# Kernel optimization log

Measured on AMD Instinct MI355X. Metric: run time of the kernel, lower is better.

## Reference

```python
import jax, jax.numpy as jnp
import numpy as np

BITS = 8
EPS = 1e-5
NUM_HEADS = 16


def ste_round(x):
    # straight-through rounding (matches brevitas round STE)
    return x + jax.lax.stop_gradient(jnp.round(x) - x)


def _scale(stat, qmax):
    return jnp.maximum(stat, 1e-8) / qmax


def fq_act_signed(x, bits=BITS):
    # runtime max-abs per-tensor scale (approximates brevitas runtime percentile 99.999)
    qmax = 2 ** (bits - 1) - 1
    qmin = -(2 ** (bits - 1))
    s = _scale(jnp.max(jnp.abs(x)), qmax)
    return jnp.clip(ste_round(x / s), qmin, qmax) * s


def fq_act_unsigned(x, bits=BITS):
    qmax = 2 ** bits - 1
    s = _scale(jnp.max(x), qmax)
    return jnp.clip(ste_round(x / s), 0, qmax) * s


def fq_weight(w, bits=BITS):
    # NarrowIntQuant + MaxStatsScaling: symmetric narrow range [-qmax, qmax]
    qmax = 2 ** (bits - 1) - 1
    s = _scale(jnp.max(jnp.abs(w)), qmax)
    return jnp.clip(ste_round(w / s), -qmax, qmax) * s


def fq_bias(b, bits=BITS):
    qmax = 2 ** (bits - 1) - 1
    qmin = -(2 ** (bits - 1))
    s = _scale(jnp.max(jnp.abs(b)), qmax)
    return jnp.clip(ste_round(b / s), qmin, qmax) * s


def layernorm(x):
    # elementwise_affine=False
    m = jnp.mean(x, axis=-1, keepdims=True)
    v = jnp.mean((x - m) ** 2, axis=-1, keepdims=True)
    return (x - m) / jnp.sqrt(v + EPS)


def setup_inputs() -> dict:
    key = jax.random.key(0)
    ks = jax.random.split(key, 13)
    B, S, E, M = 4, 1024, 1024, 4096
    std = 0.02
    inp = {
        "x": jax.random.normal(ks[0], (B, S, E), jnp.float32),
        "Wq": jax.random.normal(ks[1], (E, E), jnp.float32) * std,
        "bq": jax.random.normal(ks[2], (E,), jnp.float32) * std,
        "Wk": jax.random.normal(ks[3], (E, E), jnp.float32) * std,
        "bk": jax.random.normal(ks[4], (E,), jnp.float32) * std,
        "Wv": jax.random.normal(ks[5], (E, E), jnp.float32) * std,
        "bv": jax.random.normal(ks[6], (E,), jnp.float32) * std,
        "Wo": jax.random.normal(ks[7], (E, E), jnp.float32) * std,
        "bo": jax.random.normal(ks[8], (E,), jnp.float32) * std,
        "W1": jax.random.normal(ks[9], (M, E), jnp.float32) * std,
        "b1": jax.random.normal(ks[10], (M,), jnp.float32) * std,
        "W2": jax.random.normal(ks[11], (E, M), jnp.float32) * std,
        "b2": jax.random.normal(ks[12], (E,), jnp.float32) * std,
    }
    return inp


def reference(x, Wq, bq, Wk, bk, Wv, bv, Wo, bo, W1, b1, W2, b2):
    B, S, E = x.shape
    H = NUM_HEADS
    D = E // H
    # causal additive mask [S, S]
    i = jnp.arange(S)
    mask = jnp.where(i[None, :] <= i[:, None], 0.0, -jnp.inf).astype(x.dtype)

    # sdp_input_quant (shared q=k=v input)
    q_in = fq_act_signed(x)

    # quantized in-proj (packed_in_proj=False -> separate q/k/v projections)
    Q = q_in @ fq_weight(Wq).T + fq_bias(bq)
    K = q_in @ fq_weight(Wk).T + fq_bias(bk)
    V = q_in @ fq_weight(Wv).T + fq_bias(bv)

    Qh = Q.reshape(B, S, H, D)
    Kh = K.reshape(B, S, H, D)
    Vh = V.reshape(B, S, H, D)

    qs = fq_act_signed(Qh / jnp.sqrt(jnp.asarray(D, x.dtype)))  # q_scaled_quant
    kq = fq_act_signed(Kh)  # k_transposed_quant (per-tensor -> transpose-invariant)
    vq = fq_act_signed(Vh)  # v_quant

    scores = jnp.einsum("bqhd,bkhd->bhqk", qs, kq) + mask  # [B,H,S,S]
    attn = fq_act_signed(jax.nn.softmax(scores, axis=-1))  # attn_output_weights_quant

    ctx = jnp.einsum("bhqk,bkhd->bqhd", attn, vq).reshape(B, S, E)
    ctx = fq_act_signed(ctx)  # out_proj_input_quant
    attn_out = ctx @ fq_weight(Wo).T + fq_bias(bo)

    # residual_sdp: QuantEltwiseAdd quantizes both inputs, then layer-norm
    x1 = layernorm(fq_act_signed(x) + fq_act_signed(attn_out))

    # MLP: QuantIdentity -> QuantLinear -> QuantReLU -> QuantLinear
    h = fq_act_signed(x1) @ fq_weight(W1).T + fq_bias(b1)
    h = fq_act_unsigned(jax.nn.relu(h))
    h = h @ fq_weight(W2).T + fq_bias(b2)

    out = layernorm(fq_act_signed(x1) + fq_act_signed(h))
    return out
```

## Files before the change

kernel.cpp:

```cpp
#include <hip/hip_runtime.h>
#include <stdint.h>
#include <stddef.h>


typedef unsigned short u16;
typedef __attribute__((ext_vector_type(4))) int   i32x4;
typedef __attribute__((ext_vector_type(4))) float f32x4;

#define DEV __device__ __forceinline__

DEV float bf2f(u16 u) { return __uint_as_float(((unsigned)u) << 16); }
DEV void atomicMaxF(float* p, float v) { atomicMax((unsigned*)p, __float_as_uint(v)); }
DEV float waveMax(float v) {
#pragma unroll
  for (int o = 32; o; o >>= 1) v = fmaxf(v, __shfl_xor(v, o, 64));
  return v;
}
DEV float waveSum(float v) {
#pragma unroll
  for (int o = 32; o; o >>= 1) v += __shfl_xor(v, o, 64);
  return v;
}
DEV int waveSumI(int v) {
#pragma unroll
  for (int o = 32; o; o >>= 1) v += __shfl_xor(v, o, 64);
  return v;
}
DEV void blockStatMax(float v, float* __restrict__ slot64, float* sred4, int flatBlk) {
  v = waveMax(v);
  const int tid = threadIdx.x;
  if ((tid & 63) == 0) sred4[tid >> 6] = v;
  __syncthreads();
  if (tid == 0) {
    float m = fmaxf(fmaxf(sred4[0], sred4[1]), fmaxf(sred4[2], sred4[3]));
    atomicMaxF(&slot64[flatBlk & 63], m);
  }
}
DEV float slotMax64(const float* __restrict__ s) {
  float m = 0.f;
#pragma unroll
  for (int i = 0; i < 64; ++i) m = fmaxf(m, s[i]);
  return m;
}
DEV f32x4 ld4(const void* p, int i4, int isf32) {
  if (isf32) return ((const f32x4*)p)[i4];
  ushort4 u = ((const ushort4*)p)[i4];
  return (f32x4){bf2f(u.x), bf2f(u.y), bf2f(u.z), bf2f(u.w)};
}
DEV void gll16(const void* g, void* l) {
  __builtin_amdgcn_global_load_lds((__attribute__((address_space(1))) void*)(g),
                                   (__attribute__((address_space(3))) void*)(l),
                                   16, 0, 0);
}
DEV unsigned ldsaddr(const void* p) {
  return (unsigned)(size_t)(__attribute__((address_space(3))) const void*)p;
}
DEV unsigned quadsel(unsigned a, unsigned b, unsigned c, unsigned d, int idx) {
  unsigned lo = (idx & 1) ? b : a;
  unsigned hi = (idx & 1) ? d : c;
  return (idx & 2) ? hi : lo;
}

__global__ void detect_f32(const u16* __restrict__ x, int* __restrict__ flag) {
  const int tid = threadIdx.x;
  int cnt = 0;
#pragma unroll
  for (int i = 0; i < 16; ++i) {
    u16 u = x[tid * 16 + i];
    if ((u & 0x7f80u) >= 0x4380u) ++cnt;
  }
  cnt = waveSumI(cnt);
  if (tid == 0) flag[0] = (cnt > 16) ? 1 : 0;
}

struct AJobs { const void* p[13]; int n4[13]; int bstart[14]; };

__global__ __launch_bounds__(256) void absmax_multi(AJobs J, float* __restrict__ M,
                                                    const int* __restrict__ flagp) {
  __shared__ float sred[4];
  const int isf32 = flagp[0];
  const int blk = blockIdx.x, tid = threadIdx.x;
  int j = 0;
  while (j < 12 && blk >= J.bstart[j + 1]) ++j;
  const int lb = blk - J.bstart[j];
  const int nb = J.bstart[j + 1] - J.bstart[j];
  float mx = 0.f;
  const void* p = J.p[j];
  for (int i = lb * 256 + tid; i < J.n4[j]; i += nb * 256) {
    f32x4 v = ld4(p, i, isf32);
    mx = fmaxf(mx, fmaxf(fmaxf(fabsf(v.x), fabsf(v.y)),
                         fmaxf(fabsf(v.z), fabsf(v.w))));
  }
  blockStatMax(mx, M + j * 64, sred, lb);
}

__global__ __launch_bounds__(256) void quant_in_signed(
    const void* __restrict__ in, int8_t* __restrict__ out,
    const float* __restrict__ mp, const int* __restrict__ flagp, int n4) {
  const int isf32 = flagp[0];
  const float s = fmaxf(slotMax64(mp), 1e-8f) / 127.0f;
  char4* op = (char4*)out;
  for (int i = blockIdx.x * 256 + threadIdx.x; i < n4; i += gridDim.x * 256) {
    f32x4 v = ld4(in, i, isf32);
    char4 q;
    q.x = (signed char)fminf(fmaxf(rintf(v.x / s), -128.f), 127.f);
    q.y = (signed char)fminf(fmaxf(rintf(v.y / s), -128.f), 127.f);
    q.z = (signed char)fminf(fmaxf(rintf(v.z / s), -128.f), 127.f);
    q.w = (signed char)fminf(fmaxf(rintf(v.w / s), -128.f), 127.f);
    op[i] = q;
  }
}

struct WJobs { const void* in[5]; int8_t* out[5]; int mslot[5]; int n4[5]; int bstart[6]; };

__global__ __launch_bounds__(256) void quant_w_multi(WJobs J, const float* __restrict__ M,
                                                     const int* __restrict__ flagp) {
  const int isf32 = flagp[0];
  const int blk = blockIdx.x, tid = threadIdx.x;
  int j = 0;
  while (j < 4 && blk >= J.bstart[j + 1]) ++j;
  const int lb = blk - J.bstart[j];
  const int nb = J.bstart[j + 1] - J.bstart[j];
  const float s = fmaxf(slotMax64(M + J.mslot[j] * 64), 1e-8f) / 127.0f;
  const void* p = J.in[j];
  char4* o = (char4*)J.out[j];
  for (int i = lb * 256 + tid; i < J.n4[j]; i += nb * 256) {
    f32x4 v = ld4(p, i, isf32);
    char4 q;
    q.x = (signed char)fminf(fmaxf(rintf(v.x / s), -127.f), 127.f);
    q.y = (signed char)fminf(fmaxf(rintf(v.y / s), -127.f), 127.f);
    q.z = (signed char)fminf(fmaxf(rintf(v.z / s), -127.f), 127.f);
    q.w = (signed char)fminf(fmaxf(rintf(v.w / s), -127.f), 127.f);
    o[i] = q;
  }
}

__global__ __launch_bounds__(256) void quant_w2_rs(
    const void* __restrict__ w2, int8_t* __restrict__ out,
    const float* __restrict__ mp, const int* __restrict__ flagp,
    int* __restrict__ rowsum) {
  const int isf32 = flagp[0];
  const int row = blockIdx.x, tid = threadIdx.x;
  const float s = fmaxf(slotMax64(mp), 1e-8f) / 127.0f;
  char4* op = (char4*)(out + (size_t)row * 4096);
  int sum = 0;
  for (int i = tid; i < 1024; i += 256) {
    f32x4 v = ld4(w2, row * 1024 + i, isf32);
    char4 q;
    q.x = (signed char)fminf(fmaxf(rintf(v.x / s), -127.f), 127.f);
    q.y = (signed char)fminf(fmaxf(rintf(v.y / s), -127.f), 127.f);
    q.z = (signed char)fminf(fmaxf(rintf(v.z / s), -127.f), 127.f);
    q.w = (signed char)fminf(fmaxf(rintf(v.w / s), -127.f), 127.f);
    op[i] = q;
    sum += (int)q.x + (int)q.y + (int)q.z + (int)q.w;
  }
  sum = waveSumI(sum);
  __shared__ int rs4[4];
  if ((tid & 63) == 0) rs4[tid >> 6] = sum;
  __syncthreads();
  if (tid == 0) rowsum[row] = rs4[0] + rs4[1] + rs4[2] + rs4[3];
}

struct BJobs { const void* in[6]; float* out[6]; int mslot[6]; int n4[6]; };

__global__ __launch_bounds__(256) void fq_bias_multi(BJobs J, const float* __restrict__ M,
                                                     const int* __restrict__ flagp) {
  const int isf32 = flagp[0];
  const int j = blockIdx.x;
  const float s = fmaxf(slotMax64(M + J.mslot[j] * 64), 1e-8f) / 127.0f;
  float* o = J.out[j];
  for (int i = threadIdx.x; i < J.n4[j]; i += 256) {
    f32x4 v = ld4(J.in[j], i, isf32);
    f32x4 r;
    r.x = fminf(fmaxf(rintf(v.x / s), -128.f), 127.f) * s;
    r.y = fminf(fmaxf(rintf(v.y / s), -128.f), 127.f) * s;
    r.z = fminf(fmaxf(rintf(v.z / s), -128.f), 127.f) * s;
    r.w = fminf(fmaxf(rintf(v.w / s), -128.f), 127.f) * s;
    *(f32x4*)(o + i * 4) = r;
  }
}

__global__ __launch_bounds__(256) void quant_f32_signed(
    const float* __restrict__ in, int8_t* __restrict__ out,
    const float* __restrict__ mp, float pre, int n4) {
  const float s = fmaxf(slotMax64(mp) * pre, 1e-8f) / 127.0f;
  const f32x4* ip = (const f32x4*)in;
  char4* op = (char4*)out;
  for (int i = blockIdx.x * 256 + threadIdx.x; i < n4; i += gridDim.x * 256) {
    f32x4 v = ip[i];
    char4 q;
    q.x = (signed char)fminf(fmaxf(rintf(v.x * pre / s), -128.f), 127.f);
    q.y = (signed char)fminf(fmaxf(rintf(v.y * pre / s), -128.f), 127.f);
    q.z = (signed char)fminf(fmaxf(rintf(v.z * pre / s), -128.f), 127.f);
    q.w = (signed char)fminf(fmaxf(rintf(v.w * pre / s), -128.f), 127.f);
    op[i] = q;
  }
}

__global__ __launch_bounds__(256) void quant_v_t(
    const float* __restrict__ V, int8_t* __restrict__ Vt,
    const float* __restrict__ mp) {
  __shared__ float tile[64][65];
  const int bh = blockIdx.x, st = blockIdx.y;
  const int b = bh >> 4, h = bh & 15;
  const int tid = threadIdx.x;
  const float s = fmaxf(slotMax64(mp), 1e-8f) / 127.0f;
  const int r = tid >> 2, c = (tid & 3) * 16;
  const float* src = V + ((size_t)(b * 1024 + st * 64 + r)) * 1024 + h * 64 + c;
#pragma unroll
  for (int g = 0; g < 4; ++g) {
    f32x4 v = *(const f32x4*)(src + g * 4);
    tile[r][c + g * 4 + 0] = v.x;
    tile[r][c + g * 4 + 1] = v.y;
    tile[r][c + g * 4 + 2] = v.z;
    tile[r][c + g * 4 + 3] = v.w;
  }
  __syncthreads();
  unsigned wds[4];
#pragma unroll
  for (int g = 0; g < 4; ++g) {
    unsigned wd = 0;
#pragma unroll
    for (int k = 0; k < 4; ++k) {
      float v = tile[c + g * 4 + k][r];
      int q = (int)fminf(fmaxf(rintf(v / s), -128.f), 127.f);
      wd |= ((unsigned)(unsigned char)(signed char)q) << (8 * k);
    }
    wds[g] = wd;
  }
  i32x4 ov = {(int)wds[0], (int)wds[1], (int)wds[2], (int)wds[3]};
  *(i32x4*)(Vt + ((size_t)((b * 16 + h) * 64 + r)) * 1024 + st * 64 + c) = ov;
}

__global__ __launch_bounds__(256) void gemm_i8(
    const int8_t* __restrict__ A, const int8_t* __restrict__ B,
    float* __restrict__ Cf, int8_t* __restrict__ Cq,
    const float* __restrict__ mA, float preA, float qmaxA,
    const float* __restrict__ mB,
    const float* __restrict__ bias, const int* __restrict__ extra,
    int relu, int mode, float* __restrict__ mOut, int K, int O) {
  __shared__ __align__(16) int8_t smem[4][16384];
  __shared__ float sred[4];
  const int tid = threadIdx.x;
  const int nb = blockIdx.x, ob = blockIdx.y;
  const int w = tid >> 6, lane = tid & 63, l15 = lane & 15, quad = lane >> 4;
  const int wr = w >> 1, wc = w & 1;
  i32x4 acc[4][4];
#pragma unroll
  for (int i = 0; i < 4; ++i)
#pragma unroll
    for (int j = 0; j < 4; ++j) acc[i][j] = (i32x4){0, 0, 0, 0};
  const int r0 = tid >> 2, c0 = (tid & 3) * 16;
  const int8_t* Ab = A + (size_t)(nb * 128) * K;
  const int8_t* Bb = B + (size_t)(ob * 128) * K;
  const int nk = K >> 6;
  const int aoffl = (wr * 64 + l15) * 64 + quad * 16;
  const int boffl = 8192 + (wc * 64 + l15) * 64 + quad * 16;
  for (int t = 0; t < 3 && t < nk; ++t) {
    const size_t kt0 = (size_t)t << 6;
    int8_t* d = smem[t];
    gll16(Ab + (size_t)r0 * K + kt0 + c0, d + tid * 16);
    gll16(Ab + (size_t)(r0 + 64) * K + kt0 + c0, d + 4096 + tid * 16);
    gll16(Bb + (size_t)r0 * K + kt0 + c0, d + 8192 + tid * 16);
    gll16(Bb + (size_t)(r0 + 64) * K + kt0 + c0, d + 12288 + tid * 16);
  }
  for (int i = 0; i < nk; ++i) {
    const int infl = nk - 1 - i;
    if (infl >= 2)      asm volatile("s_waitcnt vmcnt(8)" ::: "memory");
    else if (infl == 1) asm volatile("s_waitcnt vmcnt(4)" ::: "memory");
    else                asm volatile("s_waitcnt vmcnt(0)" ::: "memory");
    asm volatile("s_barrier" ::: "memory");
    if (i + 3 < nk) {
      const size_t kt0 = (size_t)(i + 3) << 6;
      int8_t* d = smem[(i + 3) & 3];
      gll16(Ab + (size_t)r0 * K + kt0 + c0, d + tid * 16);
      gll16(Ab + (size_t)(r0 + 64) * K + kt0 + c0, d + 4096 + tid * 16);
      gll16(Bb + (size_t)r0 * K + kt0 + c0, d + 8192 + tid * 16);
      gll16(Bb + (size_t)(r0 + 64) * K + kt0 + c0, d + 12288 + tid * 16);
    }
    const unsigned a_addr = ldsaddr(smem[i & 3] + aoffl);
    const unsigned b_addr = ldsaddr(smem[i & 3] + boffl);
    i32x4 af[4], bf[4];
    asm volatile("ds_read_b128 %0, %1 offset:0"    : "=v"(af[0]) : "v"(a_addr));
    asm volatile("ds_read_b128 %0, %1 offset:1024" : "=v"(af[1]) : "v"(a_addr));
    asm volatile("ds_read_b128 %0, %1 offset:2048" : "=v"(af[2]) : "v"(a_addr));
    asm volatile("ds_read_b128 %0, %1 offset:3072" : "=v"(af[3]) : "v"(a_addr));
    asm volatile("ds_read_b128 %0, %1 offset:0"    : "=v"(bf[0]) : "v"(b_addr));
    asm volatile("ds_read_b128 %0, %1 offset:1024" : "=v"(bf[1]) : "v"(b_addr));
    asm volatile("ds_read_b128 %0, %1 offset:2048" : "=v"(bf[2]) : "v"(b_addr));
    asm volatile("ds_read_b128 %0, %1 offset:3072" : "=v"(bf[3]) : "v"(b_addr));
    asm volatile("s_waitcnt lgkmcnt(0)" ::: "memory");
    __builtin_amdgcn_sched_barrier(0);
#pragma unroll
    for (int mt = 0; mt < 4; ++mt)
#pragma unroll
      for (int nt = 0; nt < 4; ++nt)
        acc[mt][nt] = __builtin_amdgcn_mfma_i32_16x16x64_i8(af[mt], bf[nt], acc[mt][nt], 0, 0, 0);
  }
  const float sA = fmaxf(slotMax64(mA) * preA, 1e-8f) / qmaxA;
  const float sB = fmaxf(slotMax64(mB), 1e-8f) / 127.0f;
  const float sAB = sA * sB;
  const float sq = (mode == 2) ? (fmaxf(slotMax64(mOut), 1e-8f) / 255.0f) : 1.0f;
  float lmax = 0.f;
#pragma unroll
  for (int mt = 0; mt < 4; ++mt) {
    const int n = nb * 128 + wr * 64 + mt * 16 + quad * 4;
#pragma unroll
    for (int nt = 0; nt < 4; ++nt) {
      const int o = ob * 128 + wc * 64 + nt * 16 + l15;
      const int ext = extra ? 128 * extra[o] : 0;
      const float bv = bias[o];
#pragma unroll
      for (int r = 0; r < 4; ++r) {
        float v = sAB * (float)(acc[mt][nt][r] + ext) + bv;
        if (relu) v = fmaxf(v, 0.f);
        if (mode == 0) Cf[(size_t)(n + r) * O + o] = v;
        else if (mode == 2) {
          int q = (int)fminf(fmaxf(rintf(v / sq), 0.f), 255.f) - 128;
          Cq[(size_t)(n + r) * O + o] = (int8_t)q;
        }
        lmax = fmaxf(lmax, fabsf(v));
      }
    }
  }
  if (mode != 2)
    blockStatMax(lmax, mOut, sred, nb + ob * gridDim.x);
}

__global__ __launch_bounds__(256, 4) void attn_fused(
    const int8_t* __restrict__ Qq, const int8_t* __restrict__ Kq,
    const int8_t* __restrict__ Vt, float* __restrict__ ctx,
    const float* __restrict__ M, float* __restrict__ mOut) {
  __shared__ __align__(16) int8_t qtile[4096];
  __shared__ __align__(16) int8_t ktile[2][4096];
  __shared__ __align__(16) int8_t vtile[2][4096];
  __shared__ float sred[4];
  const int tid = threadIdx.x, bid = blockIdx.x;
  const int pidx = bid & 7, rh = (bid >> 3) & 1, h = (bid >> 4) & 15, b = bid >> 8;
  const int qthi = 15 - pidx, qtlo = pidx, ktmax = qthi;
  const int w = tid >> 6, lane = tid & 63, l15 = lane & 15, quad = lane >> 4;
  const int wqt = (w < 2) ? qthi : qtlo;
  const int wrow0 = rh * 32 + (w & 1) * 16;
  const float sqs = fmaxf(slotMax64(M + 13 * 64) * 0.125f, 1e-8f) / 127.0f;
  const float sk = fmaxf(slotMax64(M + 14 * 64), 1e-8f) / 127.0f;
  const float sv = fmaxf(slotMax64(M + 15 * 64), 1e-8f) / 127.0f;
  const float sqk = sqs * sk;
  const float s_attn = 1.0f / 127.0f;
  const int r0 = tid >> 2, c0 = (tid & 3) * 16;
  const int8_t* Kbase = Kq + (size_t)(b * 1024) * 1024 + h * 64 + c0;
  const int8_t* Vbase = Vt + (size_t)((b * 16 + h) * 64 + r0) * 1024 + c0;

  {
    const int qt_s = (r0 < 32) ? qthi : qtlo;
    const int qrow_g = qt_s * 64 + rh * 32 + (r0 & 31);
    gll16(Qq + ((size_t)(b * 1024 + qrow_g)) * 1024 + h * 64 + c0, qtile + tid * 16);
  }
  gll16(Kbase + (size_t)r0 * 1024, ktile[0] + tid * 16);
  __syncthreads();
  const i32x4 aq = *(const i32x4*)(qtile + (w * 16 + l15) * 64 + quad * 16);
  const int qrow = wqt * 64 + wrow0 + l15;

  float m_l = -1e30f, l_l = 0.f;
  for (int kt = 0; kt <= ktmax; ++kt) {
    if (kt) __syncthreads();
    if (kt < ktmax)
      gll16(Kbase + (size_t)((kt + 1) * 64 + r0) * 1024, ktile[(kt + 1) & 1] + tid * 16);
    if (kt <= wqt) {
      const int8_t* kc = ktile[kt & 1];
      const int kc0 = kt * 64 + quad * 4;
      float sc[4][4];
#pragma unroll
      for (int nt = 0; nt < 4; ++nt) {
        i32x4 z = {0, 0, 0, 0};
        i32x4 bk = *(const i32x4*)(kc + (nt * 16 + l15) * 64 + quad * 16);
        i32x4 d = __builtin_amdgcn_mfma_i32_16x16x64_i8(bk, aq, z, 0, 0, 0);
        if (kt == wqt) {
#pragma unroll
          for (int r = 0; r < 4; ++r)
            sc[nt][r] = (kc0 + nt * 16 + r <= qrow) ? sqk * (float)d[r] : -1e30f;
        } else {
#pragma unroll
          for (int r = 0; r < 4; ++r) sc[nt][r] = sqk * (float)d[r];
        }
      }
      float vm = sc[0][0];
#pragma unroll
      for (int nt = 0; nt < 4; ++nt)
#pragma unroll
        for (int r = 0; r < 4; ++r) vm = fmaxf(vm, sc[nt][r]);
      const float mn = fmaxf(m_l, vm);
      float sum = 0.f;
#pragma unroll
      for (int nt = 0; nt < 4; ++nt)
#pragma unroll
        for (int r = 0; r < 4; ++r) sum += __expf(sc[nt][r] - mn);
      l_l = l_l * __expf(m_l - mn) + sum;
      m_l = mn;
    }
  }
#pragma unroll
  for (int off = 16; off <= 32; off <<= 1) {
    float om = __shfl_xor(m_l, off, 64);
    float ol = __shfl_xor(l_l, off, 64);
    float mn = fmaxf(m_l, om);
    l_l = l_l * __expf(m_l - mn) + ol * __expf(om - mn);
    m_l = mn;
  }
  const float rl127 = 127.0f / l_l;

  __syncthreads();
  gll16(Kbase + (size_t)r0 * 1024, ktile[0] + tid * 16);
  gll16(Vbase, vtile[0] + tid * 16);
  i32x4 cacc[4] = {{0, 0, 0, 0}, {0, 0, 0, 0}, {0, 0, 0, 0}, {0, 0, 0, 0}};
  for (int kt = 0; kt <= ktmax; ++kt) {
    __syncthreads();
    if (kt < ktmax) {
      gll16(Kbase + (size_t)((kt + 1) * 64 + r0) * 1024, ktile[(kt + 1) & 1] + tid * 16);
      gll16(Vbase + (kt + 1) * 64, vtile[(kt + 1) & 1] + tid * 16);
    }
    if (kt <= wqt) {
      const int8_t* kc = ktile[kt & 1];
      const int kc0 = kt * 64 + quad * 4;
      unsigned Dw[4];
#pragma unroll
      for (int nt = 0; nt < 4; ++nt) {
        i32x4 z = {0, 0, 0, 0};
        i32x4 bk = *(const i32x4*)(kc + (nt * 16 + l15) * 64 + quad * 16);
        i32x4 d = __builtin_amdgcn_mfma_i32_16x16x64_i8(bk, aq, z, 0, 0, 0);
        unsigned wd = 0;
        if (kt == wqt) {
#pragma unroll
          for (int r = 0; r < 4; ++r) {
            float e = (kc0 + nt * 16 + r <= qrow)
                          ? __expf(sqk * (float)d[r] - m_l) * rl127 : 0.f;
            wd |= ((unsigned)(int)rintf(e)) << (8 * r);
          }
        } else {
#pragma unroll
          for (int r = 0; r < 4; ++r) {
            float e = __expf(sqk * (float)d[r] - m_l) * rl127;
            wd |= ((unsigned)(int)rintf(e)) << (8 * r);
          }
        }
        Dw[nt] = wd;
      }
      unsigned selfv = quadsel(Dw[0], Dw[1], Dw[2], Dw[3], quad);
      unsigned rv1 = (unsigned)__shfl_xor(
          (int)quadsel(Dw[0], Dw[1], Dw[2], Dw[3], quad ^ 1), 16, 64);
      unsigned rv2 = (unsigned)__shfl_xor(
          (int)quadsel(Dw[0], Dw[1], Dw[2], Dw[3], quad ^ 2), 32, 64);
      unsigned rv3 = (unsigned)__shfl_xor(
          (int)quadsel(Dw[0], Dw[1], Dw[2], Dw[3], quad ^ 3), 48, 64);
      i32x4 pf;
#pragma unroll
      for (int j = 0; j < 4; ++j) {
        const int t = j ^ quad;
        pf[j] = (int)((t == 0) ? selfv : (t == 1) ? rv1 : (t == 2) ? rv2 : rv3);
      }
      const int8_t* vc = vtile[kt & 1];
#pragma unroll
      for (int nt = 0; nt < 4; ++nt) {
        i32x4 bv = *(const i32x4*)(vc + (nt * 16 + l15) * 64 + quad * 16);
        cacc[nt] = __builtin_amdgcn_mfma_i32_16x16x64_i8(pf, bv, cacc[nt], 0, 0, 0);
      }
    }
  }
  const float sc2 = s_attn * sv;
  float lmax = 0.f;
  const int orow0 = wqt * 64 + wrow0 + quad * 4;
#pragma unroll
  for (int nt = 0; nt < 4; ++nt) {
    const int d = nt * 16 + l15;
#pragma unroll
    for (int r = 0; r < 4; ++r) {
      float v = sc2 * (float)cacc[nt][r];
      ctx[((size_t)(b * 1024 + orow0 + r)) * 1024 + h * 64 + d] = v;
      lmax = fmaxf(lmax, fabsf(v));
    }
  }
  blockStatMax(lmax, mOut, sred, bid);
}

__global__ __launch_bounds__(256) void ln_res(
    const int8_t* __restrict__ xq, const float* __restrict__ mx,
    const float* __restrict__ ao, const float* __restrict__ ma,
    float* __restrict__ x1, float* __restrict__ mOut) {
  __shared__ float red[8];
  __shared__ float sred[4];
  const int row = blockIdx.x, tid = threadIdx.x;
  const float sx = fmaxf(slotMax64(mx), 1e-8f) / 127.0f;
  const float sa = fmaxf(slotMax64(ma), 1e-8f) / 127.0f;
  char4 xv = *(const char4*)(xq + (size_t)row * 1024 + tid * 4);
  f32x4 av = *(const f32x4*)(ao + (size_t)row * 1024 + tid * 4);
  float t[4];
  t[0] = (float)xv.x * sx + fminf(fmaxf(rintf(av.x / sa), -128.f), 127.f) * sa;
  t[1] = (float)xv.y * sx + fminf(fmaxf(rintf(av.y / sa), -128.f), 127.f) * sa;
  t[2] = (float)xv.z * sx + fminf(fmaxf(rintf(av.z / sa), -128.f), 127.f) * sa;
  t[3] = (float)xv.w * sx + fminf(fmaxf(rintf(av.w / sa), -128.f), 127.f) * sa;
  float s = waveSum(t[0] + t[1] + t[2] + t[3]);
  if ((tid & 63) == 0) red[tid >> 6] = s;
  __syncthreads();
  const float mean = (red[0] + red[1] + red[2] + red[3]) * (1.0f / 1024.0f);
  float vs = 0.f;
#pragma unroll
  for (int i = 0; i < 4; ++i) { float d = t[i] - mean; vs += d * d; }
  vs = waveSum(vs);
  if ((tid & 63) == 0) red[4 + (tid >> 6)] = vs;
  __syncthreads();
  const float var = (red[4] + red[5] + red[6] + red[7]) * (1.0f / 1024.0f);
  const float rs = sqrtf(var + 1e-5f);
  f32x4 o;
  o.x = (t[0] - mean) / rs;
  o.y = (t[1] - mean) / rs;
  o.z = (t[2] - mean) / rs;
  o.w = (t[3] - mean) / rs;
  *(f32x4*)(x1 + (size_t)row * 1024 + tid * 4) = o;
  float lmax = fmaxf(fmaxf(fabsf(o.x), fabsf(o.y)), fmaxf(fabsf(o.z), fabsf(o.w)));
  blockStatMax(lmax, mOut, sred, row);
}

__global__ __launch_bounds__(256) void ln_final(
    const int8_t* __restrict__ x1q, const float* __restrict__ mx1,
    const float* __restrict__ h2, const float* __restrict__ mh2,
    float* __restrict__ out) {
  __shared__ float red[8];
  const int row = blockIdx.x, tid = threadIdx.x;
  const float s1 = fmaxf(slotMax64(mx1), 1e-8f) / 127.0f;
  const float s2 = fmaxf(slotMax64(mh2), 1e-8f) / 127.0f;
  char4 xv = *(const char4*)(x1q + (size_t)row * 1024 + tid * 4);
  f32x4 hv = *(const f32x4*)(h2 + (size_t)row * 1024 + tid * 4);
  float t[4];
  t[0] = (float)xv.x * s1 + fminf(fmaxf(rintf(hv.x / s2), -128.f), 127.f) * s2;
  t[1] = (float)xv.y * s1 + fminf(fmaxf(rintf(hv.y / s2), -128.f), 127.f) * s2;
  t[2] = (float)xv.z * s1 + fminf(fmaxf(rintf(hv.z / s2), -128.f), 127.f) * s2;
  t[3] = (float)xv.w * s1 + fminf(fmaxf(rintf(hv.w / s2), -128.f), 127.f) * s2;
  float s = waveSum(t[0] + t[1] + t[2] + t[3]);
  if ((tid & 63) == 0) red[tid >> 6] = s;
  __syncthreads();
  const float mean = (red[0] + red[1] + red[2] + red[3]) * (1.0f / 1024.0f);
  float vs = 0.f;
#pragma unroll
  for (int i = 0; i < 4; ++i) { float d = t[i] - mean; vs += d * d; }
  vs = waveSum(vs);
  if ((tid & 63) == 0) red[4 + (tid >> 6)] = vs;
  __syncthreads();
  const float var = (red[4] + red[5] + red[6] + red[7]) * (1.0f / 1024.0f);
  const float rs = sqrtf(var + 1e-5f);
  f32x4 o;
  o.x = (t[0] - mean) / rs;
  o.y = (t[1] - mean) / rs;
  o.z = (t[2] - mean) / rs;
  o.w = (t[3] - mean) / rs;
  *(f32x4*)(out + (size_t)row * 1024 + tid * 4) = o;
}

static constexpr size_t MB = 1u << 20;
static constexpr size_t OFF_M     = 0;
static constexpr size_t OFF_FLAG  = 6400;
static constexpr size_t OFF_BIASQ = 8192;
static constexpr size_t OFF_BIASK = OFF_BIASQ + 4096;
static constexpr size_t OFF_BIASV = OFF_BIASK + 4096;
static constexpr size_t OFF_BIASO = OFF_BIASV + 4096;
static constexpr size_t OFF_BIAS1 = OFF_BIASO + 4096;
static constexpr size_t OFF_BIAS2 = OFF_BIAS1 + 16384;
static constexpr size_t OFF_RS    = OFF_BIAS2 + 4096;
static constexpr size_t OFF_XQ    = 65536;
static constexpr size_t OFF_WQQ   = OFF_XQ  + 4 * MB;
static constexpr size_t OFF_WKQ   = OFF_WQQ + 1 * MB;
static constexpr size_t OFF_WVQ   = OFF_WKQ + 1 * MB;
static constexpr size_t OFF_WOQ   = OFF_WVQ + 1 * MB;
static constexpr size_t OFF_W1Q   = OFF_WOQ + 1 * MB;
static constexpr size_t OFF_W2Q   = OFF_W1Q + 4 * MB;
static constexpr size_t OFF_X1Q   = OFF_W2Q + 4 * MB;
static constexpr size_t OFF_A1    = OFF_X1Q + 4 * MB;
static constexpr size_t OFF_A2    = OFF_A1 + 16 * MB;

extern "C" void kernel_launch(void* const* d_in, const int* in_sizes, int n_in,
                              void* d_out, int out_size, void* d_ws, size_t ws_size,
                              hipStream_t stream) {
  (void)n_in; (void)out_size; (void)ws_size;
  char* ws = (char*)d_ws;
  float* M = (float*)(ws + OFF_M);
  int* FLAG = (int*)(ws + OFF_FLAG);
  float* BIASQ = (float*)(ws + OFF_BIASQ);
  float* BIASK = (float*)(ws + OFF_BIASK);
  float* BIASV = (float*)(ws + OFF_BIASV);
  float* BIASO = (float*)(ws + OFF_BIASO);
  float* BIAS1 = (float*)(ws + OFF_BIAS1);
  float* BIAS2 = (float*)(ws + OFF_BIAS2);
  int* RS = (int*)(ws + OFF_RS);
  int8_t* XQ  = (int8_t*)(ws + OFF_XQ);
  int8_t* WQQ = (int8_t*)(ws + OFF_WQQ);
  int8_t* WKQ = (int8_t*)(ws + OFF_WKQ);
  int8_t* WVQ = (int8_t*)(ws + OFF_WVQ);
  int8_t* WOQ = (int8_t*)(ws + OFF_WOQ);
  int8_t* W1Q = (int8_t*)(ws + OFF_W1Q);
  int8_t* W2Q = (int8_t*)(ws + OFF_W2Q);
  int8_t* X1Q = (int8_t*)(ws + OFF_X1Q);
  int8_t* QQ   = (int8_t*)(ws + OFF_A1);
  int8_t* KQQ  = (int8_t*)(ws + OFF_A1 + 4 * MB);
  int8_t* VT   = (int8_t*)(ws + OFF_A1 + 8 * MB);
  int8_t* CTXQ = (int8_t*)(ws + OFF_A1 + 12 * MB);
  float*  X1F  = (float*)(ws + OFF_A1);
  int8_t* HQ   = (int8_t*)(ws + OFF_A1);
  float* FBUF = (float*)(ws + OFF_A2);

  hipMemsetAsync(M, 0, 8192, stream);
  detect_f32<<<1, 64, 0, stream>>>((const u16*)d_in[0], FLAG);

  AJobs aj;
  const int ablk[13] = {512, 128, 1, 128, 1, 128, 1, 128, 1, 512, 2, 512, 1};
  int bs = 0;
  for (int i = 0; i < 13; ++i) {
    aj.p[i] = d_in[i];
    aj.n4[i] = in_sizes[i] / 4;
    aj.bstart[i] = bs;
    bs += ablk[i];
  }
  aj.bstart[13] = bs;
  absmax_multi<<<bs, 256, 0, stream>>>(aj, M, FLAG);

  quant_in_signed<<<1024, 256, 0, stream>>>(d_in[0], XQ, M + 0 * 64, FLAG, in_sizes[0] / 4);

  WJobs wj;
  const int widx[5] = {1, 3, 5, 7, 9};
  int8_t* wout[5] = {WQQ, WKQ, WVQ, WOQ, W1Q};
  const int wblk[5] = {128, 128, 128, 128, 512};
  int wb = 0;
  for (int j = 0; j < 5; ++j) {
    wj.in[j] = d_in[widx[j]];
    wj.out[j] = wout[j];
    wj.mslot[j] = widx[j];
    wj.n4[j] = in_sizes[widx[j]] / 4;
    wj.bstart[j] = wb;
    wb += wblk[j];
  }
  wj.bstart[5] = wb;
  quant_w_multi<<<wb, 256, 0, stream>>>(wj, M, FLAG);
  quant_w2_rs<<<1024, 256, 0, stream>>>(d_in[11], W2Q, M + 11 * 64, FLAG, RS);

  BJobs bj;
  const int bidx[6] = {2, 4, 6, 8, 10, 12};
  float* bout[6] = {BIASQ, BIASK, BIASV, BIASO, BIAS1, BIAS2};
  for (int j = 0; j < 6; ++j) {
    bj.in[j] = d_in[bidx[j]];
    bj.out[j] = bout[j];
    bj.mslot[j] = bidx[j];
    bj.n4[j] = in_sizes[bidx[j]] / 4;
  }
  fq_bias_multi<<<6, 256, 0, stream>>>(bj, M, FLAG);

  gemm_i8<<<dim3(32, 8), 256, 0, stream>>>(XQ, WQQ, FBUF, nullptr, M + 0 * 64, 1.f, 127.f, M + 1 * 64, BIASQ, nullptr, 0, 0, M + 13 * 64, 1024, 1024);
  quant_f32_signed<<<2048, 256, 0, stream>>>(FBUF, QQ, M + 13 * 64, 0.125f, 1024 * 1024);
  gemm_i8<<<dim3(32, 8), 256, 0, stream>>>(XQ, WKQ, FBUF, nullptr, M + 0 * 64, 1.f, 127.f, M + 3 * 64, BIASK, nullptr, 0, 0, M + 14 * 64, 1024, 1024);
  quant_f32_signed<<<2048, 256, 0, stream>>>(FBUF, KQQ, M + 14 * 64, 1.0f, 1024 * 1024);
  gemm_i8<<<dim3(32, 8), 256, 0, stream>>>(XQ, WVQ, FBUF, nullptr, M + 0 * 64, 1.f, 127.f, M + 5 * 64, BIASV, nullptr, 0, 0, M + 15 * 64, 1024, 1024);
  quant_v_t<<<dim3(64, 16), 256, 0, stream>>>(FBUF, VT, M + 15 * 64);

  attn_fused<<<1024, 256, 0, stream>>>(QQ, KQQ, VT, FBUF, M, M + 16 * 64);
  quant_f32_signed<<<2048, 256, 0, stream>>>(FBUF, CTXQ, M + 16 * 64, 1.0f, 1024 * 1024);

  gemm_i8<<<dim3(32, 8), 256, 0, stream>>>(CTXQ, WOQ, FBUF, nullptr, M + 16 * 64, 1.f, 127.f, M + 7 * 64, BIASO, nullptr, 0, 0, M + 17 * 64, 1024, 1024);

  ln_res<<<4096, 256, 0, stream>>>(XQ, M + 0 * 64, FBUF, M + 17 * 64, X1F, M + 18 * 64);
  quant_f32_signed<<<2048, 256, 0, stream>>>(X1F, X1Q, M + 18 * 64, 1.0f, 1024 * 1024);

  gemm_i8<<<dim3(32, 32), 256, 0, stream>>>(X1Q, W1Q, nullptr, nullptr, M + 18 * 64, 1.f, 127.f, M + 9 * 64, BIAS1, nullptr, 1, 1, M + 19 * 64, 1024, 4096);
  gemm_i8<<<dim3(32, 32), 256, 0, stream>>>(X1Q, W1Q, nullptr, HQ,      M + 18 * 64, 1.f, 127.f, M + 9 * 64, BIAS1, nullptr, 1, 2, M + 19 * 64, 1024, 4096);

  gemm_i8<<<dim3(32, 8), 256, 0, stream>>>(HQ, W2Q, FBUF, nullptr, M + 19 * 64, 1.f, 255.f, M + 11 * 64, BIAS2, RS, 0, 0, M + 20 * 64, 4096, 1024);

  ln_final<<<4096, 256, 0, stream>>>(X1Q, M + 18 * 64, FBUF, M + 20 * 64, (float*)d_out);
}
```

Baseline: 437.8 us.

## Deepen attention K/V prefetch to four-stage ring with explicit waitcnt barriers

Turns the attention kernel's double-buffered K and V LDS tiles into a four-slot ring, so loads run three tiles ahead. Each iteration syncs through explicit vmcnt waits and a raw s_barrier instead of __syncthreads. Shared-memory fragments are loaded with batched inline ds_read_b128 instructions followed by a single lgkmcnt wait. The aim is to hide global-load latency and cut barrier stalls, at the cost of doubling K/V LDS use (about 36KB per block) and relying on hand-counted vmcnt values.

```diff
diff --git a/kernel.cpp b/kernel.cpp
--- a/kernel.cpp
+++ b/kernel.cpp
@@ -332,8 +332,8 @@
     const int8_t* __restrict__ Vt, float* __restrict__ ctx,
     const float* __restrict__ M, float* __restrict__ mOut) {
   __shared__ __align__(16) int8_t qtile[4096];
-  __shared__ __align__(16) int8_t ktile[2][4096];
-  __shared__ __align__(16) int8_t vtile[2][4096];
+  __shared__ __align__(16) int8_t ktile[4][4096];
+  __shared__ __align__(16) int8_t vtile[4][4096];
   __shared__ float sred[4];
   const int tid = threadIdx.x, bid = blockIdx.x;
   const int pidx = bid & 7, rh = (bid >> 3) & 1, h = (bid >> 4) & 15, b = bid >> 8;
@@ -349,31 +349,49 @@
   const int r0 = tid >> 2, c0 = (tid & 3) * 16;
   const int8_t* Kbase = Kq + (size_t)(b * 1024) * 1024 + h * 64 + c0;
   const int8_t* Vbase = Vt + (size_t)((b * 16 + h) * 64 + r0) * 1024 + c0;
+  const unsigned fragoff = (unsigned)(l15 * 64 + quad * 16);
 
   {
     const int qt_s = (r0 < 32) ? qthi : qtlo;
     const int qrow_g = qt_s * 64 + rh * 32 + (r0 & 31);
     gll16(Qq + ((size_t)(b * 1024 + qrow_g)) * 1024 + h * 64 + c0, qtile + tid * 16);
   }
-  gll16(Kbase + (size_t)r0 * 1024, ktile[0] + tid * 16);
-  __syncthreads();
-  const i32x4 aq = *(const i32x4*)(qtile + (w * 16 + l15) * 64 + quad * 16);
+#pragma unroll
+  for (int t = 0; t < 3; ++t)
+    gll16(Kbase + (size_t)(t * 64 + r0) * 1024, ktile[t] + tid * 16);
+  asm volatile("s_waitcnt vmcnt(3)" ::: "memory");
+  asm volatile("s_barrier" ::: "memory");
+  i32x4 aq;
+  {
+    const unsigned qa = ldsaddr(qtile) + (unsigned)((w * 16 + l15) * 64 + quad * 16);
+    asm volatile("ds_read_b128 %0, %1 offset:0" : "=v"(aq) : "v"(qa));
+    asm volatile("s_waitcnt lgkmcnt(0)" ::: "memory");
+  }
   const int qrow = wqt * 64 + wrow0 + l15;
 
   float m_l = -1e30f, l_l = 0.f;
   for (int kt = 0; kt <= ktmax; ++kt) {
-    if (kt) __syncthreads();
-    if (kt < ktmax)
-      gll16(Kbase + (size_t)((kt + 1) * 64 + r0) * 1024, ktile[(kt + 1) & 1] + tid * 16);
+    if (kt + 2 <= ktmax)      asm volatile("s_waitcnt vmcnt(2)" ::: "memory");
+    else if (kt + 1 <= ktmax) asm volatile("s_waitcnt vmcnt(1)" ::: "memory");
+    else                      asm volatile("s_waitcnt vmcnt(0)" ::: "memory");
+    asm volatile("s_barrier" ::: "memory");
+    if (kt + 3 <= ktmax)
+      gll16(Kbase + (size_t)((kt + 3) * 64 + r0) * 1024, ktile[(kt + 3) & 3] + tid * 16);
     if (kt <= wqt) {
-      const int8_t* kc = ktile[kt & 1];
+      const unsigned ka = ldsaddr(ktile[kt & 3]) + fragoff;
+      i32x4 bk[4];
+      asm volatile("ds_read_b128 %0, %1 offset:0"    : "=v"(bk[0]) : "v"(ka));
+      asm volatile("ds_read_b128 %0, %1 offset:1024" : "=v"(bk[1]) : "v"(ka));
+      asm volatile("ds_read_b128 %0, %1 offset:2048" : "=v"(bk[2]) : "v"(ka));
+      asm volatile("ds_read_b128 %0, %1 offset:3072" : "=v"(bk[3]) : "v"(ka));
+      asm volatile("s_waitcnt lgkmcnt(0)" ::: "memory");
+      __builtin_amdgcn_sched_barrier(0);
       const int kc0 = kt * 64 + quad * 4;
       float sc[4][4];
 #pragma unroll
       for (int nt = 0; nt < 4; ++nt) {
         i32x4 z = {0, 0, 0, 0};
-        i32x4 bk = *(const i32x4*)(kc + (nt * 16 + l15) * 64 + quad * 16);
-        i32x4 d = __builtin_amdgcn_mfma_i32_16x16x64_i8(bk, aq, z, 0, 0, 0);
+        i32x4 d = __builtin_amdgcn_mfma_i32_16x16x64_i8(bk[nt], aq, z, 0, 0, 0);
         if (kt == wqt) {
 #pragma unroll
           for (int r = 0; r < 4; ++r)
@@ -409,24 +427,41 @@
   const float rl127 = 127.0f / l_l;
 
   __syncthreads();
-  gll16(Kbase + (size_t)r0 * 1024, ktile[0] + tid * 16);
-  gll16(Vbase, vtile[0] + tid * 16);
+#pragma unroll
+  for (int t = 0; t < 3; ++t) {
+    gll16(Kbase + (size_t)(t * 64 + r0) * 1024, ktile[t] + tid * 16);
+    gll16(Vbase + t * 64, vtile[t] + tid * 16);
+  }
   i32x4 cacc[4] = {{0, 0, 0, 0}, {0, 0, 0, 0}, {0, 0, 0, 0}, {0, 0, 0, 0}};
   for (int kt = 0; kt <= ktmax; ++kt) {
-    __syncthreads();
-    if (kt < ktmax) {
-      gll16(Kbase + (size_t)((kt + 1) * 64 + r0) * 1024, ktile[(kt + 1) & 1] + tid * 16);
-      gll16(Vbase + (kt + 1) * 64, vtile[(kt + 1) & 1] + tid * 16);
+    if (kt + 2 <= ktmax)      asm volatile("s_waitcnt vmcnt(4)" ::: "memory");
+    else if (kt + 1 <= ktmax) asm volatile("s_waitcnt vmcnt(2)" ::: "memory");
+    else                      asm volatile("s_waitcnt vmcnt(0)" ::: "memory");
+    asm volatile("s_barrier" ::: "memory");
+    if (kt + 3 <= ktmax) {
+      gll16(Kbase + (size_t)((kt + 3) * 64 + r0) * 1024, ktile[(kt + 3) & 3] + tid * 16);
+      gll16(Vbase + (kt + 3) * 64, vtile[(kt + 3) & 3] + tid * 16);
     }
     if (kt <= wqt) {
-      const int8_t* kc = ktile[kt & 1];
+      const unsigned ka = ldsaddr(ktile[kt & 3]) + fragoff;
+      const unsigned va = ldsaddr(vtile[kt & 3]) + fragoff;
+      i32x4 bk[4], bv[4];
+      asm volatile("ds_read_b128 %0, %1 offset:0"    : "=v"(bk[0]) : "v"(ka));
+      asm volatile("ds_read_b128 %0, %1 offset:1024" : "=v"(bk[1]) : "v"(ka));
+      asm volatile("ds_read_b128 %0, %1 offset:2048" : "=v"(bk[2]) : "v"(ka));
+      asm volatile("ds_read_b128 %0, %1 offset:3072" : "=v"(bk[3]) : "v"(ka));
+      asm volatile("ds_read_b128 %0, %1 offset:0"    : "=v"(bv[0]) : "v"(va));
+      asm volatile("ds_read_b128 %0, %1 offset:1024" : "=v"(bv[1]) : "v"(va));
+      asm volatile("ds_read_b128 %0, %1 offset:2048" : "=v"(bv[2]) : "v"(va));
+      asm volatile("ds_read_b128 %0, %1 offset:3072" : "=v"(bv[3]) : "v"(va));
+      asm volatile("s_waitcnt lgkmcnt(0)" ::: "memory");
+      __builtin_amdgcn_sched_barrier(0);
       const int kc0 = kt * 64 + quad * 4;
       unsigned Dw[4];
 #pragma unroll
       for (int nt = 0; nt < 4; ++nt) {
         i32x4 z = {0, 0, 0, 0};
-        i32x4 bk = *(const i32x4*)(kc + (nt * 16 + l15) * 64 + quad * 16);
-        i32x4 d = __builtin_amdgcn_mfma_i32_16x16x64_i8(bk, aq, z, 0, 0, 0);
+        i32x4 d = __builtin_amdgcn_mfma_i32_16x16x64_i8(bk[nt], aq, z, 0, 0, 0);
         unsigned wd = 0;
         if (kt == wqt) {
 #pragma unroll
@@ -457,12 +492,9 @@
         const int t = j ^ quad;
         pf[j] = (int)((t == 0) ? selfv : (t == 1) ? rv1 : (t == 2) ? rv2 : rv3);
       }
-      const int8_t* vc = vtile[kt & 1];
-#pragma unroll
-      for (int nt = 0; nt < 4; ++nt) {
-        i32x4 bv = *(const i32x4*)(vc + (nt * 16 + l15) * 64 + quad * 16);
-        cacc[nt] = __builtin_amdgcn_mfma_i32_16x16x64_i8(pf, bv, cacc[nt], 0, 0, 0);
-      }
+#pragma unroll
+      for (int nt = 0; nt < 4; ++nt)
+        cacc[nt] = __builtin_amdgcn_mfma_i32_16x16x64_i8(pf, bv[nt], cacc[nt], 0, 0, 0);
     }
   }
   const float sc2 = s_attn * sv;
```

Result: no change. 432.9 us (-1.1%).
